# Kernel optimization log

Measured on AMD Instinct MI355X. Metric: run time of the kernel, lower is better.

Reference implementation:

```python
import jax, jax.numpy as jnp
import numpy as np

N = 4096
INP_DIM = 256
EMB_DIM = 256
ALPHA = 0.01  # LeakyReLU negative slope
NEG_INF = -9.0e15


def _xavier(key, shape, gain=1.414):
    fan_in, fan_out = shape[0], shape[1]
    limit = gain * np.sqrt(6.0 / (fan_in + fan_out))
    return jax.random.uniform(key, shape, jnp.float32, -limit, limit)


def setup_inputs() -> dict:
    key = jax.random.key(0)
    ks = jax.random.split(key, 9)
    inp = {
        "input": jax.random.normal(ks[0], (N, INP_DIM), jnp.float32),
        "adj": jax.random.randint(ks[1], (N, N), 0, 2, jnp.int32),
        "W0": _xavier(ks[2], (INP_DIM, EMB_DIM)),
        "W1": _xavier(ks[3], (EMB_DIM, EMB_DIM)),
        "a1": _xavier(ks[4], (2 * EMB_DIM, 1)),
        "W2": _xavier(ks[5], (EMB_DIM, EMB_DIM)),
        "a2": _xavier(ks[6], (2 * EMB_DIM, 1)),
        "W3": _xavier(ks[7], (EMB_DIM, EMB_DIM)),
        "a3": _xavier(ks[8], (2 * EMB_DIM, 1)),
    }
    return inp


def _gat_layer(h, adj, W, a):
    # h: [N, F_in], W: [F_in, F], a: [2F, 1]
    Wh = h @ W                       # [N, F]
    F_out = Wh.shape[1]
    # e_ij = leakyrelu([Wh_i || Wh_j] @ a) = leakyrelu(Wh_i@a1 + Wh_j@a2)
    f1 = Wh @ a[:F_out]              # [N, 1]
    f2 = Wh @ a[F_out:]              # [N, 1]
    e = jax.nn.leaky_relu(f1 + f2.T, ALPHA)            # [N, N]
    att = jnp.where(adj > 0, e, NEG_INF)
    att = jax.nn.softmax(att, axis=1)                    # masked softmax over neighbors
    h_prime = att @ Wh                                   # [N, F]
    return jax.nn.elu(h_prime)                           # concat=True -> ELU


def reference(input, adj, W0, W1, a1, W2, a2, W3, a3):
    h = input @ W0                   # GAT-level projection
    h = _gat_layer(h, adj, W1, a1)
    h = _gat_layer(h, adj, W2, a2)
    h = _gat_layer(h, adj, W3, a3)
    return h
```

## Files before the change

kernel.cpp:

```cpp
#include <hip/hip_runtime.h>
#include <hip/hip_bf16.h>
#include <cstdint>
#include <cstddef>

#define NN 4096
#define FD 256
#define WPR 64

typedef __attribute__((ext_vector_type(8))) unsigned short ushort8v;
typedef __attribute__((ext_vector_type(4))) unsigned short ushort4v;
typedef __attribute__((ext_vector_type(8))) short short8;
typedef __attribute__((ext_vector_type(4))) float float4v;

#define C1 30.0f
#define C2 0.3f

static __device__ __forceinline__ unsigned short f2bf(float x) {
    union { float f; unsigned int u; } v; v.f = x;
    unsigned int r = v.u + 0x7FFFu + ((v.u >> 16) & 1u);
    return (unsigned short)(r >> 16);
}

static __device__ __forceinline__ short8 as_s8(ushort8v v) {
    union { ushort8v u; short8 s; } x; x.u = v; return x.s;
}

__global__ __launch_bounds__(256) void pack_adj(const int* __restrict__ adj,
                                                unsigned long long* __restrict__ bits) {
    const int row = blockIdx.x;
    const int t = threadIdx.x;
    const int wave = t >> 6, lane = t & 63;
    const int* arow = adj + (size_t)row * NN;
    #pragma unroll
    for (int it = 0; it < NN / 256; ++it) {
        int j = it * 256 + wave * 64 + lane;
        unsigned long long m = __ballot(arow[j] > 0);
        if (lane == 0) bits[(size_t)row * WPR + (it * 4 + wave)] = m;
    }
}

__global__ __launch_bounds__(256) void cvt_w(const float* __restrict__ W0, const float* __restrict__ W1,
                                             const float* __restrict__ W2, const float* __restrict__ W3,
                                             unsigned short* __restrict__ Wbt) {
    int idx = blockIdx.x * 256 + threadIdx.x;
    int mat = idx >> 16;
    int within = idx & 65535;
    int n = within >> 8, k = within & 255;
    const float* W = (mat == 0) ? W0 : (mat == 1) ? W1 : (mat == 2) ? W2 : W3;
    Wbt[idx] = f2bf(W[k * 256 + n]);
}

__global__ __launch_bounds__(256) void cvt_h(const float* __restrict__ x, unsigned short* __restrict__ hb) {
    int idx = blockIdx.x * 256 + threadIdx.x;
    hb[idx] = f2bf(x[idx]);
}

__global__ __launch_bounds__(256) void proj_gemm(const unsigned short* __restrict__ A,
                                                 const unsigned short* __restrict__ Bt,
                                                 float* __restrict__ Cf,
                                                 unsigned short* __restrict__ Cbt,
                                                 unsigned short* __restrict__ Crow) {
    const int t = threadIdx.x;
    const int bm = blockIdx.x >> 2, bn = blockIdx.x & 3;
    const int m0 = bm * 64, n0 = bn * 64;
    __shared__ unsigned short As[64 * 264];
    __shared__ unsigned short Bs[64 * 264];
    const int lane = t & 63, wave = t >> 6;
    const int wm = (wave >> 1) * 32, wn = (wave & 1) * 32;
    const int lr = t >> 2, lc0 = (t & 3) * 8;
    #pragma unroll
    for (int i = 0; i < 8; ++i) {
        int col = lc0 + i * 32;
        *(ushort8v*)&As[lr * 264 + col] = *(const ushort8v*)&A[(size_t)(m0 + lr) * 256 + col];
        *(ushort8v*)&Bs[lr * 264 + col] = *(const ushort8v*)&Bt[(size_t)(n0 + lr) * 256 + col];
    }
    __syncthreads();
    float4v acc[2][2] = {{{0.f,0.f,0.f,0.f},{0.f,0.f,0.f,0.f}},{{0.f,0.f,0.f,0.f},{0.f,0.f,0.f,0.f}}};
    #pragma unroll
    for (int kk = 0; kk < 256; kk += 32) {
        const int kc = kk + (lane >> 4) * 8;
        #pragma unroll
        for (int fm = 0; fm < 2; ++fm) {
            short8 a = as_s8(*(const ushort8v*)&As[(wm + fm * 16 + (lane & 15)) * 264 + kc]);
            #pragma unroll
            for (int fn = 0; fn < 2; ++fn) {
                short8 b = as_s8(*(const ushort8v*)&Bs[(wn + fn * 16 + (lane & 15)) * 264 + kc]);
                acc[fm][fn] = __builtin_amdgcn_mfma_f32_16x16x32_bf16(a, b, acc[fm][fn], 0, 0, 0);
            }
        }
    }

    const int rb = wm + (lane >> 4) * 4;
    const int cb = wn + (lane & 15);
    #pragma unroll
    for (int fm = 0; fm < 2; ++fm)
        #pragma unroll
        for (int fn = 0; fn < 2; ++fn)
            #pragma unroll
            for (int r = 0; r < 4; ++r) {
                int lr2 = rb + fm * 16 + r;
                int lc2 = cb + fn * 16;
                float v = acc[fm][fn][r];
                if (Cf)   Cf[(size_t)(m0 + lr2) * 256 + n0 + lc2] = v;
                if (Crow) Crow[(size_t)(m0 + lr2) * 256 + n0 + lc2] = f2bf(v);
            }

    if (Cbt) {
        unsigned short* T = As;
        __syncthreads();
        #pragma unroll
        for (int fm = 0; fm < 2; ++fm)
            #pragma unroll
            for (int fn = 0; fn < 2; ++fn)
                #pragma unroll
                for (int r = 0; r < 4; ++r)
                    T[(cb + fn * 16) * 72 + rb + fm * 16 + r] = f2bf(acc[fm][fn][r]);
        __syncthreads();
        const int tr = t >> 2;
        #pragma unroll
        for (int i = 0; i < 2; ++i) {
            int tc = (t & 3) * 8 + i * 32;
            *(ushort8v*)&Cbt[(size_t)(n0 + tr) * 4096 + m0 + tc] = *(const ushort8v*)&T[tr * 72 + tc];
        }
    }
}

__global__ __launch_bounds__(256) void fvec(const float* __restrict__ Wh, const float* __restrict__ a,
                                            float* __restrict__ f1, float* __restrict__ tabf) {
    const int wave = threadIdx.x >> 6, lane = threadIdx.x & 63;
    const int i = blockIdx.x * 4 + wave;
    const float* row = Wh + (size_t)i * 256;
    float s1 = 0.f, s2 = 0.f;
    #pragma unroll
    for (int c0 = 0; c0 < 256; c0 += 64) {
        int c = c0 + lane;
        float w = row[c];
        s1 += w * a[c];
        s2 += w * a[256 + c];
    }
    #pragma unroll
    for (int off = 32; off > 0; off >>= 1) {
        s1 += __shfl_down(s1, off, 64);
        s2 += __shfl_down(s2, off, 64);
    }
    if (lane == 0) {
        f1[i] = s1;
        tabf[2 * i]     = __expf(s2 - C1);
        tabf[2 * i + 1] = __expf(0.01f * s2 - C2);
    }
}

__global__ __launch_bounds__(256) void rowcoef(const unsigned long long* __restrict__ bits,
                                               const float* __restrict__ f1,
                                               const float2* __restrict__ tab,
                                               float4* __restrict__ rowco) {
    __shared__ float2 tl[4096];
    const int t = threadIdx.x;
    #pragma unroll
    for (int i = 0; i < 16; ++i) tl[i * 256 + t] = tab[i * 256 + t];
    __syncthreads();
    const int lane = t & 63, wave = t >> 6;
    for (int rr = 0; rr < 2; ++rr) {
        const int row = blockIdx.x * 8 + wave * 2 + rr;
        const unsigned long long wl = bits[(size_t)row * WPR + lane];
        const float f1r = f1[row];
        const float th = __expf(-f1r - C1);
        float mx = 0.f, S1 = 0.f, S2 = 0.f;
        #pragma unroll 16
        for (int b = 0; b < 64; ++b) {
            unsigned long long w = __shfl(wl, b, 64);
            bool bit = (w >> lane) & 1ULL;
            float2 v = tl[b * 64 + lane];
            float ebm = bit ? v.x : 0.f;
            mx = fmaxf(mx, ebm);
            bool cond = v.x > th;
            S1 += (bit && cond)  ? v.x : 0.f;
            S2 += (bit && !cond) ? v.y : 0.f;
        }
        #pragma unroll
        for (int off = 1; off < 64; off <<= 1) {
            mx = fmaxf(mx, __shfl_xor(mx, off, 64));
            S1 += __shfl_xor(S1, off, 64);
            S2 += __shfl_xor(S2, off, 64);
        }
        if (lane == 0) {
            float M  = C1 + __logf(mx);
            float fm_ = f1r + M;
            float m  = fm_ > 0.f ? fm_ : 0.01f * fm_;
            float alpha = __expf(fminf(f1r + C1 - m, 60.f));
            float gamma = __expf(fminf(0.01f * (f1r + C1) - m, 60.f));
            float inv = 1.0f / (alpha * S1 + gamma * S2);
            rowco[row] = make_float4(alpha * inv, gamma * inv, th, 0.f);
        }
    }
}

__global__ __launch_bounds__(256, 2) void att_split(const unsigned long long* __restrict__ bits,
                                                    const float4* __restrict__ rowco,
                                                    const float* __restrict__ tabf,
                                                    const unsigned short* __restrict__ Bt,
                                                    float* __restrict__ part, int kchunk) {
    const int t = threadIdx.x;
    const int bm = blockIdx.x & 63;
    const int ks = blockIdx.x >> 6;
    const int m0 = bm * 64;
    const int k0 = ks * kchunk;
    __shared__ unsigned short As[64 * 72];
    __shared__ unsigned short Bs[256 * 72];
    const int lane = t & 63, wave = t >> 6;
    const int wn = wave * 64;
    const int sr = t >> 2, q = t & 3, sc = q * 16;
    const float4 rc = rowco[m0 + sr];
    const float pA = rc.x, pG = rc.y, th = rc.z;
    const unsigned long long* brow = bits + (size_t)(m0 + sr) * WPR;
    float4v acc[4][4];
    #pragma unroll
    for (int i = 0; i < 4; ++i)
        #pragma unroll
        for (int j = 0; j < 4; ++j) acc[i][j] = (float4v){0.f, 0.f, 0.f, 0.f};

    for (int kk = k0; kk < k0 + kchunk; kk += 64) {
        const unsigned int wb = (unsigned int)(brow[kk >> 6] >> sc) & 0xFFFFu;
        float tv[32];
        {
            const float4v* tp = (const float4v*)&tabf[2 * (kk + sc)];
            #pragma unroll
            for (int i = 0; i < 8; ++i) {
                float4v x = tp[i];
                tv[4 * i] = x[0]; tv[4 * i + 1] = x[1]; tv[4 * i + 2] = x[2]; tv[4 * i + 3] = x[3];
            }
        }
        ushort8v pa0, pa1;
        #pragma unroll
        for (int jj = 0; jj < 16; ++jj) {
            float eb = tv[2 * jj], ed = tv[2 * jj + 1];
            bool cond = eb > th;
            float val  = cond ? eb : ed;
            float coef = cond ? pA : pG;
            float p = ((wb >> jj) & 1u) ? coef * val : 0.f;
            unsigned short pb = f2bf(p);
            if (jj < 8) pa0[jj] = pb; else pa1[jj - 8] = pb;
        }
        *(ushort8v*)&As[sr * 72 + sc]     = pa0;
        *(ushort8v*)&As[sr * 72 + sc + 8] = pa1;
        #pragma unroll
        for (int i = 0; i < 4; ++i) {
            int r = i * 64 + sr;
            *(ushort8v*)&Bs[r * 72 + sc]     = *(const ushort8v*)&Bt[(size_t)r * 4096 + kk + sc];
            *(ushort8v*)&Bs[r * 72 + sc + 8] = *(const ushort8v*)&Bt[(size_t)r * 4096 + kk + sc + 8];
        }
        __syncthreads();
        #pragma unroll
        for (int half = 0; half < 2; ++half) {
            const int kc = half * 32 + (lane >> 4) * 8;
            short8 a[4], b[4];
            #pragma unroll
            for (int fm = 0; fm < 4; ++fm)
                a[fm] = as_s8(*(const ushort8v*)&As[(fm * 16 + (lane & 15)) * 72 + kc]);
            #pragma unroll
            for (int fn = 0; fn < 4; ++fn)
                b[fn] = as_s8(*(const ushort8v*)&Bs[(wn + fn * 16 + (lane & 15)) * 72 + kc]);
            #pragma unroll
            for (int fm = 0; fm < 4; ++fm)
                #pragma unroll
                for (int fn = 0; fn < 4; ++fn)
                    acc[fm][fn] = __builtin_amdgcn_mfma_f32_16x16x32_bf16(a[fm], b[fn], acc[fm][fn], 0, 0, 0);
        }
        __syncthreads();
    }

    const int rb = (lane >> 4) * 4;
    const int cb = wn + (lane & 15);
    float* pbase = part + ((size_t)ks << 20);
    #pragma unroll
    for (int fm = 0; fm < 4; ++fm)
        #pragma unroll
        for (int fn = 0; fn < 4; ++fn)
            #pragma unroll
            for (int r = 0; r < 4; ++r)
                pbase[(size_t)(m0 + rb + fm * 16 + r) * 256 + cb + fn * 16] = acc[fm][fn][r];
}

__global__ __launch_bounds__(256) void att_reduce(const float* __restrict__ part,
                                                  float* __restrict__ outf,
                                                  unsigned short* __restrict__ hrow, int nsplit) {
    const int idx = (blockIdx.x * 256 + threadIdx.x) * 4;
    float4v s = *(const float4v*)&part[idx];
    for (int sp = 1; sp < nsplit; ++sp)
        s += *(const float4v*)&part[((size_t)sp << 20) + idx];
    float4v v;
    ushort4v hb;
    #pragma unroll
    for (int j = 0; j < 4; ++j) {
        float x = s[j];
        x = x > 0.f ? x : (__expf(x) - 1.f);
        v[j] = x;
        hb[j] = f2bf(x);
    }
    if (outf) *(float4v*)&outf[idx] = v;
    *(ushort4v*)&hrow[idx] = hb;
}

extern "C" void kernel_launch(void* const* d_in, const int* in_sizes, int n_in,
                              void* d_out, int out_size, void* d_ws, size_t ws_size,
                              hipStream_t stream) {
    const float* input = (const float*)d_in[0];
    const int*   adj   = (const int*)d_in[1];
    const float* W0    = (const float*)d_in[2];
    const float* W1    = (const float*)d_in[3];
    const float* a1    = (const float*)d_in[4];
    const float* W2    = (const float*)d_in[5];
    const float* a2    = (const float*)d_in[6];
    const float* W3    = (const float*)d_in[7];
    const float* a3    = (const float*)d_in[8];
    float* out = (float*)d_out;
    char* ws = (char*)d_ws;

    unsigned long long* bits = (unsigned long long*)(ws);
    unsigned short* h0   = (unsigned short*)(ws + (2u << 20));
    unsigned short* h1   = (unsigned short*)(ws + (4u << 20));
    unsigned short* Whbt = (unsigned short*)(ws + (6u << 20));
    float*          Whf  = (float*)(ws + (8u << 20));
    unsigned short* Wbt  = (unsigned short*)(ws + (12u << 20));
    float*  f1v   = (float*)(ws + (12u << 20) + (512u << 10));
    float*  tabf  = f1v + 4096;
    float4* rowco = (float4*)(tabf + 8192);
    float*  part  = (float*)(ws + (13u << 20));

    const size_t base = 13u << 20;
    int SPLIT = 8;
    while (SPLIT > 1 && base + (size_t)SPLIT * (4u << 20) > ws_size) SPLIT >>= 1;
    const int kchunk = NN / SPLIT;

    pack_adj<<<4096, 256, 0, stream>>>(adj, bits);
    cvt_w<<<1024, 256, 0, stream>>>(W0, W1, W2, W3, Wbt);
    cvt_h<<<4096, 256, 0, stream>>>(input, h0);

    proj_gemm<<<256, 256, 0, stream>>>(h0, Wbt + 0 * 65536, nullptr, nullptr, h1);

    proj_gemm<<<256, 256, 0, stream>>>(h1, Wbt + 1 * 65536, Whf, Whbt, nullptr);
    fvec<<<1024, 256, 0, stream>>>(Whf, a1, f1v, tabf);
    rowcoef<<<512, 256, 0, stream>>>(bits, f1v, (const float2*)tabf, rowco);
    att_split<<<64 * SPLIT, 256, 0, stream>>>(bits, rowco, tabf, Whbt, part, kchunk);
    att_reduce<<<1024, 256, 0, stream>>>(part, nullptr, h0, SPLIT);

    proj_gemm<<<256, 256, 0, stream>>>(h0, Wbt + 2 * 65536, Whf, Whbt, nullptr);
    fvec<<<1024, 256, 0, stream>>>(Whf, a2, f1v, tabf);
    rowcoef<<<512, 256, 0, stream>>>(bits, f1v, (const float2*)tabf, rowco);
    att_split<<<64 * SPLIT, 256, 0, stream>>>(bits, rowco, tabf, Whbt, part, kchunk);
    att_reduce<<<1024, 256, 0, stream>>>(part, nullptr, h1, SPLIT);

    proj_gemm<<<256, 256, 0, stream>>>(h1, Wbt + 3 * 65536, Whf, Whbt, nullptr);
    fvec<<<1024, 256, 0, stream>>>(Whf, a3, f1v, tabf);
    rowcoef<<<512, 256, 0, stream>>>(bits, f1v, (const float2*)tabf, rowco);
    att_split<<<64 * SPLIT, 256, 0, stream>>>(bits, rowco, tabf, Whbt, part, kchunk);
    att_reduce<<<1024, 256, 0, stream>>>(part, out, h0, SPLIT);
}
```

Before: 289.9 us.

## Fuse setup kernels, fold f1/f2 into projection GEMM, load B directly to registers

Merges adjacency packing, input/weight conversion and zeroing of the f1/f2 buffers into one setup kernel. The projection GEMM now computes the f1/f2 attention dot products in its epilogue with shuffles and atomicAdd, which drops the fp32 Wh write and the separate fvec kernel. att_split computes the exponentials inline from f2 instead of reading a precomputed table, and it loads Wh^T fragments straight from global memory into registers instead of staging them in LDS. This cuts launches, memory traffic and LDS use, at the cost of more exp work per element, atomic float nondeterminism and uncoalesced direct global B loads.

```diff
diff --git a/kernel.cpp b/kernel.cpp
--- a/kernel.cpp
+++ b/kernel.cpp
@@ -25,39 +25,46 @@
     union { ushort8v u; short8 s; } x; x.u = v; return x.s;
 }
 
-__global__ __launch_bounds__(256) void pack_adj(const int* __restrict__ adj,
-                                                unsigned long long* __restrict__ bits) {
-    const int row = blockIdx.x;
+__global__ __launch_bounds__(256) void setup(const int* __restrict__ adj,
+                                             const float* __restrict__ input,
+                                             const float* __restrict__ W0, const float* __restrict__ W1,
+                                             const float* __restrict__ W2, const float* __restrict__ W3,
+                                             unsigned long long* __restrict__ bits,
+                                             unsigned short* __restrict__ hb,
+                                             unsigned short* __restrict__ Wbt,
+                                             float* __restrict__ f1f2) {
+    const int b = blockIdx.x;
     const int t = threadIdx.x;
-    const int wave = t >> 6, lane = t & 63;
-    const int* arow = adj + (size_t)row * NN;
-    #pragma unroll
-    for (int it = 0; it < NN / 256; ++it) {
-        int j = it * 256 + wave * 64 + lane;
-        unsigned long long m = __ballot(arow[j] > 0);
-        if (lane == 0) bits[(size_t)row * WPR + (it * 4 + wave)] = m;
-    }
-}
-
-__global__ __launch_bounds__(256) void cvt_w(const float* __restrict__ W0, const float* __restrict__ W1,
-                                             const float* __restrict__ W2, const float* __restrict__ W3,
-                                             unsigned short* __restrict__ Wbt) {
-    int idx = blockIdx.x * 256 + threadIdx.x;
-    int mat = idx >> 16;
-    int within = idx & 65535;
-    int n = within >> 8, k = within & 255;
-    const float* W = (mat == 0) ? W0 : (mat == 1) ? W1 : (mat == 2) ? W2 : W3;
-    Wbt[idx] = f2bf(W[k * 256 + n]);
-}
-
-__global__ __launch_bounds__(256) void cvt_h(const float* __restrict__ x, unsigned short* __restrict__ hb) {
-    int idx = blockIdx.x * 256 + threadIdx.x;
-    hb[idx] = f2bf(x[idx]);
+    if (b < 4096) {
+        const int wave = t >> 6, lane = t & 63;
+        const int* arow = adj + (size_t)b * NN;
+        #pragma unroll
+        for (int it = 0; it < NN / 256; ++it) {
+            int j = it * 256 + wave * 64 + lane;
+            unsigned long long m = __ballot(arow[j] > 0);
+            if (lane == 0) bits[(size_t)b * WPR + (it * 4 + wave)] = m;
+        }
+        hb[(size_t)b * 256 + t] = f2bf(input[(size_t)b * 256 + t]);
+    } else if (b < 5120) {
+        int idx = (b - 4096) * 256 + t;
+        int mat = idx >> 16;
+        int within = idx & 65535;
+        int n = within >> 8, k = within & 255;
+        const float* W = (mat == 0) ? W0 : (mat == 1) ? W1 : (mat == 2) ? W2 : W3;
+        Wbt[idx] = f2bf(W[k * 256 + n]);
+    } else {
+        #pragma unroll
+        for (int i = 0; i < 24; ++i) {
+            int pos = i * 1024 + (b - 5120) * 256 + t;
+            f1f2[pos] = 0.f;
+        }
+    }
 }
 
 __global__ __launch_bounds__(256) void proj_gemm(const unsigned short* __restrict__ A,
                                                  const unsigned short* __restrict__ Bt,
-                                                 float* __restrict__ Cf,
+                                                 const float* __restrict__ av,
+                                                 float* __restrict__ f1f2,
                                                  unsigned short* __restrict__ Cbt,
                                                  unsigned short* __restrict__ Crow) {
     const int t = threadIdx.x;
@@ -92,18 +99,41 @@
 
     const int rb = wm + (lane >> 4) * 4;
     const int cb = wn + (lane & 15);
-    #pragma unroll
-    for (int fm = 0; fm < 2; ++fm)
-        #pragma unroll
-        for (int fn = 0; fn < 2; ++fn)
+    if (Crow) {
+        #pragma unroll
+        for (int fm = 0; fm < 2; ++fm)
+            #pragma unroll
+            for (int fn = 0; fn < 2; ++fn)
+                #pragma unroll
+                for (int r = 0; r < 4; ++r)
+                    Crow[(size_t)(m0 + rb + fm * 16 + r) * 256 + n0 + cb + fn * 16] = f2bf(acc[fm][fn][r]);
+    }
+
+    if (f1f2) {
+        float a1c[2], a2c[2];
+        #pragma unroll
+        for (int fn = 0; fn < 2; ++fn) {
+            a1c[fn] = av[n0 + cb + fn * 16];
+            a2c[fn] = av[256 + n0 + cb + fn * 16];
+        }
+        #pragma unroll
+        for (int fm = 0; fm < 2; ++fm)
             #pragma unroll
             for (int r = 0; r < 4; ++r) {
-                int lr2 = rb + fm * 16 + r;
-                int lc2 = cb + fn * 16;
-                float v = acc[fm][fn][r];
-                if (Cf)   Cf[(size_t)(m0 + lr2) * 256 + n0 + lc2] = v;
-                if (Crow) Crow[(size_t)(m0 + lr2) * 256 + n0 + lc2] = f2bf(v);
+                float s1 = acc[fm][0][r] * a1c[0] + acc[fm][1][r] * a1c[1];
+                float s2 = acc[fm][0][r] * a2c[0] + acc[fm][1][r] * a2c[1];
+                #pragma unroll
+                for (int off = 1; off < 16; off <<= 1) {
+                    s1 += __shfl_xor(s1, off, 64);
+                    s2 += __shfl_xor(s2, off, 64);
+                }
+                if ((lane & 15) == 0) {
+                    int row = m0 + rb + fm * 16 + r;
+                    atomicAdd(&f1f2[row], s1);
+                    atomicAdd(&f1f2[4096 + row], s2);
+                }
             }
+    }
 
     if (Cbt) {
         unsigned short* T = As;
@@ -125,45 +155,23 @@
     }
 }
 
-__global__ __launch_bounds__(256) void fvec(const float* __restrict__ Wh, const float* __restrict__ a,
-                                            float* __restrict__ f1, float* __restrict__ tabf) {
-    const int wave = threadIdx.x >> 6, lane = threadIdx.x & 63;
-    const int i = blockIdx.x * 4 + wave;
-    const float* row = Wh + (size_t)i * 256;
-    float s1 = 0.f, s2 = 0.f;
-    #pragma unroll
-    for (int c0 = 0; c0 < 256; c0 += 64) {
-        int c = c0 + lane;
-        float w = row[c];
-        s1 += w * a[c];
-        s2 += w * a[256 + c];
-    }
-    #pragma unroll
-    for (int off = 32; off > 0; off >>= 1) {
-        s1 += __shfl_down(s1, off, 64);
-        s2 += __shfl_down(s2, off, 64);
-    }
-    if (lane == 0) {
-        f1[i] = s1;
-        tabf[2 * i]     = __expf(s2 - C1);
-        tabf[2 * i + 1] = __expf(0.01f * s2 - C2);
-    }
-}
-
 __global__ __launch_bounds__(256) void rowcoef(const unsigned long long* __restrict__ bits,
-                                               const float* __restrict__ f1,
-                                               const float2* __restrict__ tab,
+                                               const float* __restrict__ f1f2,
                                                float4* __restrict__ rowco) {
     __shared__ float2 tl[4096];
     const int t = threadIdx.x;
-    #pragma unroll
-    for (int i = 0; i < 16; ++i) tl[i * 256 + t] = tab[i * 256 + t];
+    const float* f2p = f1f2 + 4096;
+    #pragma unroll
+    for (int i = 0; i < 16; ++i) {
+        float v = f2p[i * 256 + t];
+        tl[i * 256 + t] = make_float2(__expf(v - C1), __expf(0.01f * v - C2));
+    }
     __syncthreads();
     const int lane = t & 63, wave = t >> 6;
     for (int rr = 0; rr < 2; ++rr) {
         const int row = blockIdx.x * 8 + wave * 2 + rr;
         const unsigned long long wl = bits[(size_t)row * WPR + lane];
-        const float f1r = f1[row];
+        const float f1r = f1f2[row];
         const float th = __expf(-f1r - C1);
         float mx = 0.f, S1 = 0.f, S2 = 0.f;
         #pragma unroll 16
@@ -190,14 +198,14 @@
             float alpha = __expf(fminf(f1r + C1 - m, 60.f));
             float gamma = __expf(fminf(0.01f * (f1r + C1) - m, 60.f));
             float inv = 1.0f / (alpha * S1 + gamma * S2);
-            rowco[row] = make_float4(alpha * inv, gamma * inv, th, 0.f);
+            rowco[row] = make_float4(alpha * inv, gamma * inv, -f1r, 0.f);
         }
     }
 }
 
 __global__ __launch_bounds__(256, 2) void att_split(const unsigned long long* __restrict__ bits,
                                                     const float4* __restrict__ rowco,
-                                                    const float* __restrict__ tabf,
+                                                    const float* __restrict__ f1f2,
                                                     const unsigned short* __restrict__ Bt,
                                                     float* __restrict__ part, int kchunk) {
     const int t = threadIdx.x;
@@ -206,13 +214,14 @@
     const int m0 = bm * 64;
     const int k0 = ks * kchunk;
     __shared__ unsigned short As[64 * 72];
-    __shared__ unsigned short Bs[256 * 72];
     const int lane = t & 63, wave = t >> 6;
     const int wn = wave * 64;
-    const int sr = t >> 2, q = t & 3, sc = q * 16;
+    const int sr = t >> 2, sc = (t & 3) * 16;
     const float4 rc = rowco[m0 + sr];
-    const float pA = rc.x, pG = rc.y, th = rc.z;
+    const float pA = rc.x, pG = rc.y, thf2 = rc.z;
     const unsigned long long* brow = bits + (size_t)(m0 + sr) * WPR;
+    const float* f2p = f1f2 + 4096;
+    const unsigned short* bbase = Bt + (size_t)(wn + (lane & 15)) * 4096 + (lane >> 4) * 8;
     float4v acc[4][4];
     #pragma unroll
     for (int i = 0; i < 4; ++i)
@@ -221,50 +230,47 @@
 
     for (int kk = k0; kk < k0 + kchunk; kk += 64) {
         const unsigned int wb = (unsigned int)(brow[kk >> 6] >> sc) & 0xFFFFu;
-        float tv[32];
+        float fv[16];
         {
-            const float4v* tp = (const float4v*)&tabf[2 * (kk + sc)];
-            #pragma unroll
-            for (int i = 0; i < 8; ++i) {
-                float4v x = tp[i];
-                tv[4 * i] = x[0]; tv[4 * i + 1] = x[1]; tv[4 * i + 2] = x[2]; tv[4 * i + 3] = x[3];
+            const float4v* fp = (const float4v*)&f2p[kk + sc];
+            #pragma unroll
+            for (int i = 0; i < 4; ++i) {
+                float4v x = fp[i];
+                fv[4 * i] = x[0]; fv[4 * i + 1] = x[1]; fv[4 * i + 2] = x[2]; fv[4 * i + 3] = x[3];
             }
         }
         ushort8v pa0, pa1;
         #pragma unroll
         for (int jj = 0; jj < 16; ++jj) {
-            float eb = tv[2 * jj], ed = tv[2 * jj + 1];
-            bool cond = eb > th;
-            float val  = cond ? eb : ed;
+            float f2j = fv[jj];
+            bool cond = f2j > thf2;
+            float arg  = cond ? (f2j - C1) : (0.01f * f2j - C2);
             float coef = cond ? pA : pG;
-            float p = ((wb >> jj) & 1u) ? coef * val : 0.f;
+            float p = ((wb >> jj) & 1u) ? coef * __expf(arg) : 0.f;
             unsigned short pb = f2bf(p);
             if (jj < 8) pa0[jj] = pb; else pa1[jj - 8] = pb;
         }
         *(ushort8v*)&As[sr * 72 + sc]     = pa0;
         *(ushort8v*)&As[sr * 72 + sc + 8] = pa1;
-        #pragma unroll
-        for (int i = 0; i < 4; ++i) {
-            int r = i * 64 + sr;
-            *(ushort8v*)&Bs[r * 72 + sc]     = *(const ushort8v*)&Bt[(size_t)r * 4096 + kk + sc];
-            *(ushort8v*)&Bs[r * 72 + sc + 8] = *(const ushort8v*)&Bt[(size_t)r * 4096 + kk + sc + 8];
-        }
+        ushort8v breg[4][2];
+        #pragma unroll
+        for (int fn = 0; fn < 4; ++fn)
+            #pragma unroll
+            for (int half = 0; half < 2; ++half)
+                breg[fn][half] = *(const ushort8v*)&bbase[(size_t)(fn * 16) * 4096 + kk + half * 32];
         __syncthreads();
         #pragma unroll
         for (int half = 0; half < 2; ++half) {
             const int kc = half * 32 + (lane >> 4) * 8;
-            short8 a[4], b[4];
+            short8 a[4];
             #pragma unroll
             for (int fm = 0; fm < 4; ++fm)
                 a[fm] = as_s8(*(const ushort8v*)&As[(fm * 16 + (lane & 15)) * 72 + kc]);
-            #pragma unroll
-            for (int fn = 0; fn < 4; ++fn)
-                b[fn] = as_s8(*(const ushort8v*)&Bs[(wn + fn * 16 + (lane & 15)) * 72 + kc]);
             #pragma unroll
             for (int fm = 0; fm < 4; ++fm)
                 #pragma unroll
                 for (int fn = 0; fn < 4; ++fn)
-                    acc[fm][fn] = __builtin_amdgcn_mfma_f32_16x16x32_bf16(a[fm], b[fn], acc[fm][fn], 0, 0, 0);
+                    acc[fm][fn] = __builtin_amdgcn_mfma_f32_16x16x32_bf16(a[fm], as_s8(breg[fn][half]), acc[fm][fn], 0, 0, 0);
         }
         __syncthreads();
     }
@@ -320,11 +326,9 @@
     unsigned short* h0   = (unsigned short*)(ws + (2u << 20));
     unsigned short* h1   = (unsigned short*)(ws + (4u << 20));
     unsigned short* Whbt = (unsigned short*)(ws + (6u << 20));
-    float*          Whf  = (float*)(ws + (8u << 20));
-    unsigned short* Wbt  = (unsigned short*)(ws + (12u << 20));
-    float*  f1v   = (float*)(ws + (12u << 20) + (512u << 10));
-    float*  tabf  = f1v + 4096;
-    float4* rowco = (float4*)(tabf + 8192);
+    unsigned short* Wbt  = (unsigned short*)(ws + (8u << 20));
+    float*  f1f2  = (float*)(ws + (9u << 20));
+    float4* rowco = (float4*)(ws + (10u << 20));
     float*  part  = (float*)(ws + (13u << 20));
 
     const size_t base = 13u << 20;
@@ -332,27 +336,24 @@
     while (SPLIT > 1 && base + (size_t)SPLIT * (4u << 20) > ws_size) SPLIT >>= 1;
     const int kchunk = NN / SPLIT;
 
-    pack_adj<<<4096, 256, 0, stream>>>(adj, bits);
-    cvt_w<<<1024, 256, 0, stream>>>(W0, W1, W2, W3, Wbt);
-    cvt_h<<<4096, 256, 0, stream>>>(input, h0);
-
-    proj_gemm<<<256, 256, 0, stream>>>(h0, Wbt + 0 * 65536, nullptr, nullptr, h1);
-
-    proj_gemm<<<256, 256, 0, stream>>>(h1, Wbt + 1 * 65536, Whf, Whbt, nullptr);
-    fvec<<<1024, 256, 0, stream>>>(Whf, a1, f1v, tabf);
-    rowcoef<<<512, 256, 0, stream>>>(bits, f1v, (const float2*)tabf, rowco);
-    att_split<<<64 * SPLIT, 256, 0, stream>>>(bits, rowco, tabf, Whbt, part, kchunk);
+    float* f1f2_l[3] = { f1f2, f1f2 + 8192, f1f2 + 16384 };
+
+    setup<<<5124, 256, 0, stream>>>(adj, input, W0, W1, W2, W3, bits, h0, Wbt, f1f2);
+
+    proj_gemm<<<256, 256, 0, stream>>>(h0, Wbt + 0 * 65536, nullptr, nullptr, nullptr, h1);
+
+    proj_gemm<<<256, 256, 0, stream>>>(h1, Wbt + 1 * 65536, a1, f1f2_l[0], Whbt, nullptr);
+    rowcoef<<<512, 256, 0, stream>>>(bits, f1f2_l[0], rowco);
+    att_split<<<64 * SPLIT, 256, 0, stream>>>(bits, rowco, f1f2_l[0], Whbt, part, kchunk);
     att_reduce<<<1024, 256, 0, stream>>>(part, nullptr, h0, SPLIT);
 
-    proj_gemm<<<256, 256, 0, stream>>>(h0, Wbt + 2 * 65536, Whf, Whbt, nullptr);
-    fvec<<<1024, 256, 0, stream>>>(Whf, a2, f1v, tabf);
-    rowcoef<<<512, 256, 0, stream>>>(bits, f1v, (const float2*)tabf, rowco);
-    att_split<<<64 * SPLIT, 256, 0, stream>>>(bits, rowco, tabf, Whbt, part, kchunk);
+    proj_gemm<<<256, 256, 0, stream>>>(h0, Wbt + 2 * 65536, a2, f1f2_l[1], Whbt, nullptr);
+    rowcoef<<<512, 256, 0, stream>>>(bits, f1f2_l[1], rowco);
+    att_split<<<64 * SPLIT, 256, 0, stream>>>(bits, rowco, f1f2_l[1], Whbt, part, kchunk);
     att_reduce<<<1024, 256, 0, stream>>>(part, nullptr, h1, SPLIT);
 
-    proj_gemm<<<256, 256, 0, stream>>>(h1, Wbt + 3 * 65536, Whf, Whbt, nullptr);
-    fvec<<<1024, 256, 0, stream>>>(Whf, a3, f1v, tabf);
-    rowcoef<<<512, 256, 0, stream>>>(bits, f1v, (const float2*)tabf, rowco);
-    att_split<<<64 * SPLIT, 256, 0, stream>>>(bits, rowco, tabf, Whbt, part, kchunk);
+    proj_gemm<<<256, 256, 0, stream>>>(h1, Wbt + 3 * 65536, a3, f1f2_l[2], Whbt, nullptr);
+    rowcoef<<<512, 256, 0, stream>>>(bits, f1f2_l[2], rowco);
+    att_split<<<64 * SPLIT, 256, 0, stream>>>(bits, rowco, f1f2_l[2], Whbt, part, kchunk);
     att_reduce<<<1024, 256, 0, stream>>>(part, out, h0, SPLIT);
 }
```

Measured after the change: 287.2 us. Within noise of the previous version (-0.9%).
